# Kernel optimization log

Measured on AMD Instinct MI355X. Metric: run time of the kernel, lower is better.

The kernel has to match this reference:

```python
import jax, jax.numpy as jnp
import numpy as np

HIDDEN = 1024
HEADS = 16
D_HEAD = HIDDEN // HEADS  # 64
N = 2048


def setup_inputs() -> dict:
    key = jax.random.key(0)
    ks = jax.random.split(key, 12)
    s = 1.0 / np.sqrt(HIDDEN)
    return {
        "q": jax.random.normal(ks[0], (N, HIDDEN), jnp.float32),
        "k": jax.random.normal(ks[1], (N, HIDDEN), jnp.float32),
        "v": jax.random.normal(ks[2], (N, HIDDEN), jnp.float32),
        "attn_bias": jax.random.normal(ks[3], (HEADS, 1, N, N), jnp.float32),
        "Wq": jax.random.normal(ks[4], (HIDDEN, HIDDEN), jnp.float32) * s,
        "bq": jax.random.normal(ks[5], (HIDDEN,), jnp.float32) * s,
        "Wk": jax.random.normal(ks[6], (HIDDEN, HIDDEN), jnp.float32) * s,
        "bk": jax.random.normal(ks[7], (HIDDEN,), jnp.float32) * s,
        "Wv": jax.random.normal(ks[8], (HIDDEN, HIDDEN), jnp.float32) * s,
        "bv": jax.random.normal(ks[9], (HIDDEN,), jnp.float32) * s,
        "Wo": jax.random.normal(ks[10], (HIDDEN, HIDDEN), jnp.float32) * s,
        "bo": jax.random.normal(ks[11], (HIDDEN,), jnp.float32) * s,
    }


def reference(q, k, v, attn_bias, Wq, bq, Wk, bk, Wv, bv, Wo, bo):
    # q,k,v: [N, hidden]; attn_bias: [H, 1, N, N]. Attention runs over the
    # node axis (dim 0 in the torch code), inner seq dim is 1 (squeezed).
    n = q.shape[0]
    scale = D_HEAD ** -0.5
    qh = (q @ Wq.T + bq).reshape(n, HEADS, D_HEAD).transpose(1, 0, 2)  # [H,N,d]
    kh = (k @ Wk.T + bk).reshape(n, HEADS, D_HEAD).transpose(1, 0, 2)  # [H,N,d]
    vh = (v @ Wv.T + bv).reshape(n, HEADS, D_HEAD).transpose(1, 0, 2)  # [H,N,d]
    scores = jnp.einsum('hnd,hmd->hnm', qh * scale, kh) + attn_bias[:, 0]  # [H,N,N]
    attn = jax.nn.softmax(scores, axis=-1)
    ctx = jnp.einsum('hnm,hmd->hnd', attn, vh)            # [H,N,d]
    ctx = ctx.transpose(1, 0, 2).reshape(n, HEADS * D_HEAD)  # [N,hidden]
    return ctx @ Wo.T + bo
```

## Files before the change

### kernel.cpp

```cpp
#include <hip/hip_runtime.h>
#include <type_traits>
#include <utility>

#define NT 2048
#define HD 1024
#define NHEAD 16
#define DHEAD 64
#define LOG2E 1.44269504f

typedef float f32x4 __attribute__((ext_vector_type(4)));
typedef __bf16 b16x8 __attribute__((ext_vector_type(8)));
typedef short s16x8 __attribute__((ext_vector_type(8)));
typedef unsigned short u16x8 __attribute__((ext_vector_type(8)));
typedef unsigned short u16x4 __attribute__((ext_vector_type(4)));

template <typename V, typename = void>
struct mfma_takes : std::false_type {};
template <typename V>
struct mfma_takes<V, std::void_t<decltype(__builtin_amdgcn_mfma_f32_16x16x32_bf16(
                         std::declval<V>(), std::declval<V>(), std::declval<f32x4>(), 0, 0, 0))>>
    : std::true_type {};

template <typename V>
__device__ __forceinline__ f32x4 mfma_impl(V a, V b, f32x4 c) {
  return __builtin_amdgcn_mfma_f32_16x16x32_bf16(a, b, c, 0, 0, 0);
}

__device__ __forceinline__ f32x4 mfma_bf16(u16x8 a, u16x8 b, f32x4 c) {
  using V = typename std::conditional<mfma_takes<b16x8>::value, b16x8, s16x8>::type;
  return mfma_impl<V>(__builtin_bit_cast(V, a), __builtin_bit_cast(V, b), c);
}

__device__ __forceinline__ unsigned short f2bf(float f) {
  unsigned int u = __builtin_bit_cast(unsigned int, f);
  return (unsigned short)((u + 0x7FFFu + ((u >> 16) & 1u)) >> 16);
}

__device__ __forceinline__ void gload16(const unsigned short* g, unsigned short* l) {
  __builtin_amdgcn_global_load_lds(
      (__attribute__((address_space(1))) void*)(void*)(g),
      (__attribute__((address_space(3))) void*)(void*)(l), 16, 0, 0);
}

__global__ __launch_bounds__(256) void cvt_bf16(
    const float* __restrict__ s0, const float* __restrict__ s1, const float* __restrict__ s2,
    const float* __restrict__ s3, const float* __restrict__ s4, const float* __restrict__ s5,
    const float* __restrict__ s6,
    unsigned short* __restrict__ d0, unsigned short* __restrict__ d1, unsigned short* __restrict__ d2,
    unsigned short* __restrict__ d3, unsigned short* __restrict__ d4, unsigned short* __restrict__ d5,
    unsigned short* __restrict__ d6) {
  const int seg = blockIdx.y;
  const float* s;
  unsigned short* d;
  switch (seg) {
    case 0: s = s0; d = d0; break;
    case 1: s = s1; d = d1; break;
    case 2: s = s2; d = d2; break;
    case 3: s = s3; d = d3; break;
    case 4: s = s4; d = d4; break;
    case 5: s = s5; d = d5; break;
    default: s = s6; d = d6; break;
  }
  const int n = (seg < 3) ? NT * HD : HD * HD;
  for (int i = blockIdx.x * 2048 + threadIdx.x * 8; i < n; i += gridDim.x * 2048) {
    f32x4 f0 = *reinterpret_cast<const f32x4*>(&s[i]);
    f32x4 f1 = *reinterpret_cast<const f32x4*>(&s[i + 4]);
    u16x8 o;
#pragma unroll
    for (int e = 0; e < 4; ++e) { o[e] = f2bf(f0[e]); o[e + 4] = f2bf(f1[e]); }
    *reinterpret_cast<u16x8*>(&d[i]) = o;
  }
}

__device__ __forceinline__ void gemm_mainloop(
    const unsigned short* __restrict__ A, const unsigned short* __restrict__ B,
    unsigned short* As, unsigned short* Bs, int n0, int m0, f32x4 acc[4][4]) {
  const int tid = threadIdx.x;
  const int lane = tid & 63;
  const int wr = (tid >> 6) >> 1, wc = (tid >> 6) & 1;
  const int srow = tid >> 3;
  const int scol = (tid & 7) << 3;

  for (int kt = 0; kt < HD; kt += 64) {
    __syncthreads();
#pragma unroll
    for (int i = 0; i < 4; ++i) {
      gload16(&A[(size_t)(n0 + srow + i * 32) * HD + kt + scol], As + i * 2048 + tid * 8);
      gload16(&B[(size_t)(m0 + srow + i * 32) * HD + kt + scol], Bs + i * 2048 + tid * 8);
    }
    __syncthreads();
#pragma unroll
    for (int ks = 0; ks < 2; ++ks) {
      const int kcol = ks * 32 + (lane >> 4) * 8;
      u16x8 a[4], b[4];
#pragma unroll
      for (int i = 0; i < 4; ++i)
        a[i] = *reinterpret_cast<const u16x8*>(&As[(wr * 64 + i * 16 + (lane & 15)) * 64 + kcol]);
#pragma unroll
      for (int j = 0; j < 4; ++j)
        b[j] = *reinterpret_cast<const u16x8*>(&Bs[(wc * 64 + j * 16 + (lane & 15)) * 64 + kcol]);
#pragma unroll
      for (int i = 0; i < 4; ++i)
#pragma unroll
        for (int j = 0; j < 4; ++j)
          acc[i][j] = mfma_bf16(a[i], b[j], acc[i][j]);
    }
  }
}

__global__ __launch_bounds__(256) void proj_gemm(
    const unsigned short* __restrict__ qb, const unsigned short* __restrict__ kb,
    const unsigned short* __restrict__ vb,
    const unsigned short* __restrict__ Wqb, const unsigned short* __restrict__ Wkb,
    const unsigned short* __restrict__ Wvb,
    const float* __restrict__ bq, const float* __restrict__ bk, const float* __restrict__ bv,
    unsigned short* __restrict__ Qh, unsigned short* __restrict__ Kh,
    unsigned short* __restrict__ Vt) {
  const int z = blockIdx.z;
  const unsigned short* A = (z == 0) ? qb : (z == 1) ? kb : vb;
  const unsigned short* B = (z == 0) ? Wqb : (z == 1) ? Wkb : Wvb;
  const float* bias = (z == 0) ? bq : (z == 1) ? bk : bv;

  __shared__ unsigned short As[128 * 64];
  __shared__ unsigned short Bs[128 * 64];

  const int n0 = blockIdx.x * 128;
  const int m0 = blockIdx.y * 128;
  const int tid = threadIdx.x;
  const int lane = tid & 63;
  const int wr = (tid >> 6) >> 1, wc = (tid >> 6) & 1;

  f32x4 acc[4][4] = {};
  gemm_mainloop(A, B, As, Bs, n0, m0, acc);

  const int rgrp = (lane >> 4) * 4;
  const float scale = (z == 0) ? 0.125f * LOG2E : 1.0f;
#pragma unroll
  for (int i = 0; i < 4; ++i) {
    const int nb = n0 + wr * 64 + i * 16 + rgrp;
#pragma unroll
    for (int j = 0; j < 4; ++j) {
      const int m = m0 + wc * 64 + j * 16 + (lane & 15);
      const float bb = bias[m];
      if (z == 2) {
        u16x4 pk;
#pragma unroll
        for (int r = 0; r < 4; ++r) pk[r] = f2bf(acc[i][j][r] + bb);
        *reinterpret_cast<u16x4*>(&Vt[(size_t)m * NT + nb]) = pk;
      } else {
        unsigned short* dst = (z == 0) ? Qh : Kh;
#pragma unroll
        for (int r = 0; r < 4; ++r)
          dst[(size_t)(nb + r) * HD + m] = f2bf((acc[i][j][r] + bb) * scale);
      }
    }
  }
}

__global__ __launch_bounds__(256) void attn_kernel(
    const unsigned short* __restrict__ Qh, const unsigned short* __restrict__ Kh,
    const unsigned short* __restrict__ Vt, const float* __restrict__ bias,
    unsigned short* __restrict__ ctx) {
  const int h = blockIdx.y;
  const int q0 = blockIdx.x * 64;
  const int tid = threadIdx.x;
  const int lane = tid & 63;
  const int wave = tid >> 6;

  __shared__ unsigned short Ks[128][72];
  __shared__ unsigned short Vs[64][136];
  __shared__ unsigned short Ps[4][16][136];

  u16x8 qf[2];
  {
    const int qrow = q0 + wave * 16 + (lane & 15);
    const int db = (lane >> 4) * 8;
    qf[0] = *reinterpret_cast<const u16x8*>(&Qh[(size_t)qrow * HD + h * DHEAD + db]);
    qf[1] = *reinterpret_cast<const u16x8*>(&Qh[(size_t)qrow * HD + h * DHEAD + 32 + db]);
  }

  f32x4 oacc[4] = {};
  float mrun[4], lrun[4];
#pragma unroll
  for (int r = 0; r < 4; ++r) { mrun[r] = -3.0e38f; lrun[r] = 0.f; }

  const float* bias_h = bias + (size_t)h * NT * NT;
  const int qlrow = q0 + wave * 16 + (lane >> 4) * 4;

  const int ksr = tid >> 3, ksc = (tid & 7) << 3;
  const int vsd = tid >> 2, vsc = (tid & 3) << 3;
  const unsigned short* Kbase = Kh + h * DHEAD;
  const unsigned short* Vbase = Vt + (size_t)(h * DHEAD + vsd) * NT;

#pragma unroll
  for (int p = 0; p < 4; ++p)
    *reinterpret_cast<u16x8*>(&Ks[ksr + p * 32][ksc]) =
        *reinterpret_cast<const u16x8*>(&Kbase[(size_t)(ksr + p * 32) * HD + ksc]);
#pragma unroll
  for (int p = 0; p < 4; ++p)
    *reinterpret_cast<u16x8*>(&Vs[vsd][vsc + p * 32]) =
        *reinterpret_cast<const u16x8*>(&Vbase[vsc + p * 32]);
  __syncthreads();

  for (int t = 0; t < NT / 128; ++t) {
    const int kt = t * 128;
    float br[8][4];
    const float* bp = bias_h + (size_t)qlrow * NT + kt + (lane & 15);
#pragma unroll
    for (int j = 0; j < 8; ++j)
#pragma unroll
      for (int r = 0; r < 4; ++r) br[j][r] = bp[(size_t)r * NT + j * 16];

    u16x8 kpre[4], vpre[4];
    const bool more = (t + 1 < NT / 128);
    if (more) {
      const int kt2 = kt + 128;
#pragma unroll
      for (int p = 0; p < 4; ++p)
        kpre[p] = *reinterpret_cast<const u16x8*>(&Kbase[(size_t)(kt2 + ksr + p * 32) * HD + ksc]);
#pragma unroll
      for (int p = 0; p < 4; ++p)
        vpre[p] = *reinterpret_cast<const u16x8*>(&Vbase[kt2 + vsc + p * 32]);
    }

    f32x4 s[8] = {};
#pragma unroll
    for (int ks = 0; ks < 2; ++ks) {
      const int kcol = ks * 32 + (lane >> 4) * 8;
#pragma unroll
      for (int j = 0; j < 8; ++j) {
        u16x8 kf = *reinterpret_cast<const u16x8*>(&Ks[j * 16 + (lane & 15)][kcol]);
        s[j] = mfma_bf16(qf[ks], kf, s[j]);
      }
    }
#pragma unroll
    for (int j = 0; j < 8; ++j)
#pragma unroll
      for (int r = 0; r < 4; ++r) s[j][r] = fmaf(br[j][r], LOG2E, s[j][r]);

    float mnew[4];
#pragma unroll
    for (int r = 0; r < 4; ++r) {
      float mx = s[0][r];
#pragma unroll
      for (int j = 1; j < 8; ++j) mx = fmaxf(mx, s[j][r]);
      mx = fmaxf(mx, __shfl_xor(mx, 1));
      mx = fmaxf(mx, __shfl_xor(mx, 2));
      mx = fmaxf(mx, __shfl_xor(mx, 4));
      mx = fmaxf(mx, __shfl_xor(mx, 8));
      mnew[r] = fmaxf(mrun[r], mx);
    }
#pragma unroll
    for (int r = 0; r < 4; ++r) {
      const float corr = exp2f(mrun[r] - mnew[r]);
      lrun[r] *= corr;
#pragma unroll
      for (int nd = 0; nd < 4; ++nd) oacc[nd][r] *= corr;
      mrun[r] = mnew[r];
    }
    float psum[4] = {0.f, 0.f, 0.f, 0.f};
#pragma unroll
    for (int j = 0; j < 8; ++j)
#pragma unroll
      for (int r = 0; r < 4; ++r) {
        const float p = exp2f(s[j][r] - mrun[r]);
        psum[r] += p;
        Ps[wave][(lane >> 4) * 4 + r][j * 16 + (lane & 15)] = f2bf(p);
      }
#pragma unroll
    for (int r = 0; r < 4; ++r) {
      float tsum = psum[r];
      tsum += __shfl_xor(tsum, 1);
      tsum += __shfl_xor(tsum, 2);
      tsum += __shfl_xor(tsum, 4);
      tsum += __shfl_xor(tsum, 8);
      lrun[r] += tsum;
    }

#pragma unroll
    for (int kk = 0; kk < 4; ++kk) {
      const int kcol = kk * 32 + (lane >> 4) * 8;
      u16x8 pa = *reinterpret_cast<const u16x8*>(&Ps[wave][lane & 15][kcol]);
#pragma unroll
      for (int nd = 0; nd < 4; ++nd) {
        u16x8 vb = *reinterpret_cast<const u16x8*>(&Vs[nd * 16 + (lane & 15)][kcol]);
        oacc[nd] = mfma_bf16(pa, vb, oacc[nd]);
      }
    }
    __syncthreads();
    if (more) {
#pragma unroll
      for (int p = 0; p < 4; ++p)
        *reinterpret_cast<u16x8*>(&Ks[ksr + p * 32][ksc]) = kpre[p];
#pragma unroll
      for (int p = 0; p < 4; ++p)
        *reinterpret_cast<u16x8*>(&Vs[vsd][vsc + p * 32]) = vpre[p];
    }
    __syncthreads();
  }

#pragma unroll
  for (int nd = 0; nd < 4; ++nd) {
#pragma unroll
    for (int r = 0; r < 4; ++r) {
      const float val = oacc[nd][r] / lrun[r];
      ctx[(size_t)(qlrow + r) * HD + h * DHEAD + nd * 16 + (lane & 15)] = f2bf(val);
    }
  }
}

__global__ __launch_bounds__(256) void out_gemm(
    const unsigned short* __restrict__ Ain, const unsigned short* __restrict__ Wob,
    const float* __restrict__ bias, float* __restrict__ out) {
  __shared__ unsigned short As[128 * 64];
  __shared__ unsigned short Bs[128 * 64];

  const int n0 = blockIdx.x * 128;
  const int m0 = blockIdx.y * 128;
  const int tid = threadIdx.x;
  const int lane = tid & 63;
  const int wr = (tid >> 6) >> 1, wc = (tid >> 6) & 1;

  f32x4 acc[4][4] = {};
  gemm_mainloop(Ain, Wob, As, Bs, n0, m0, acc);

  const int rgrp = (lane >> 4) * 4;
#pragma unroll
  for (int i = 0; i < 4; ++i) {
    const int nb = n0 + wr * 64 + i * 16 + rgrp;
#pragma unroll
    for (int j = 0; j < 4; ++j) {
      const int m = m0 + wc * 64 + j * 16 + (lane & 15);
      const float bb = bias[m];
#pragma unroll
      for (int r = 0; r < 4; ++r)
        out[(size_t)(nb + r) * HD + m] = acc[i][j][r] + bb;
    }
  }
}

extern "C" void kernel_launch(void* const* d_in, const int* in_sizes, int n_in,
                              void* d_out, int out_size, void* d_ws, size_t ws_size,
                              hipStream_t stream) {
  const float* q  = (const float*)d_in[0];
  const float* k  = (const float*)d_in[1];
  const float* v  = (const float*)d_in[2];
  const float* ab = (const float*)d_in[3];
  const float* Wq = (const float*)d_in[4];
  const float* bq = (const float*)d_in[5];
  const float* Wk = (const float*)d_in[6];
  const float* bk = (const float*)d_in[7];
  const float* Wv = (const float*)d_in[8];
  const float* bv = (const float*)d_in[9];
  const float* Wo = (const float*)d_in[10];
  const float* bo = (const float*)d_in[11];

  unsigned short* qb  = (unsigned short*)d_ws;
  unsigned short* kb  = qb + (size_t)NT * HD;
  unsigned short* vb  = kb + (size_t)NT * HD;
  unsigned short* Wqb = vb + (size_t)NT * HD;
  unsigned short* Wkb = Wqb + (size_t)HD * HD;
  unsigned short* Wvb = Wkb + (size_t)HD * HD;
  unsigned short* Wob = Wvb + (size_t)HD * HD;
  unsigned short* Qh  = Wob + (size_t)HD * HD;
  unsigned short* Kh  = Qh + (size_t)NT * HD;
  unsigned short* Vt  = Kh + (size_t)NT * HD;
  unsigned short* ctx = Vt + (size_t)NT * HD;

  cvt_bf16<<<dim3(512, 7), 256, 0, stream>>>(q, k, v, Wq, Wk, Wv, Wo,
                                             qb, kb, vb, Wqb, Wkb, Wvb, Wob);
  proj_gemm<<<dim3(NT / 128, HD / 128, 3), 256, 0, stream>>>(
      qb, kb, vb, Wqb, Wkb, Wvb, bq, bk, bv, Qh, Kh, Vt);
  attn_kernel<<<dim3(NT / 64, NHEAD), 256, 0, stream>>>(Qh, Kh, Vt, ab, ctx);
  out_gemm<<<dim3(NT / 128, HD / 128), 256, 0, stream>>>(ctx, Wob, bo, (float*)d_out);
}
```

Measured before the change: 147.4 us.

## Double-buffer GEMM mainloop with 64x128 tiles and XCD-aware block mapping

Shrinks the projection and output GEMM tiles to 64x128 and double-buffers shared memory, so the next K-slice loads while the current one computes and there is one barrier per slice. This doubles block count for better occupancy on the many-CU GPU. Grids are flattened to 1D with remapped indices: the GEMMs group blocks by weight column tile, and attention assigns two heads per XCD so each XCD's L2 reuses the same K/V. Costs are more shared memory per block, and the smaller tiles need more A/B traffic per output.

```diff
diff --git a/kernel.cpp b/kernel.cpp
--- a/kernel.cpp
+++ b/kernel.cpp
@@ -72,39 +72,55 @@
   }
 }
 
-__device__ __forceinline__ void gemm_mainloop(
+__device__ __forceinline__ void gemm64x128(
     const unsigned short* __restrict__ A, const unsigned short* __restrict__ B,
-    unsigned short* As, unsigned short* Bs, int n0, int m0, f32x4 acc[4][4]) {
+    int n0, int m0,
+    unsigned short* As0, unsigned short* As1,
+    unsigned short* Bs0, unsigned short* Bs1, f32x4 acc[2][4]) {
   const int tid = threadIdx.x;
   const int lane = tid & 63;
   const int wr = (tid >> 6) >> 1, wc = (tid >> 6) & 1;
   const int srow = tid >> 3;
   const int scol = (tid & 7) << 3;
 
-  for (int kt = 0; kt < HD; kt += 64) {
-    __syncthreads();
-#pragma unroll
-    for (int i = 0; i < 4; ++i) {
-      gload16(&A[(size_t)(n0 + srow + i * 32) * HD + kt + scol], As + i * 2048 + tid * 8);
-      gload16(&B[(size_t)(m0 + srow + i * 32) * HD + kt + scol], Bs + i * 2048 + tid * 8);
-    }
-    __syncthreads();
+  auto stage = [&](int kt, unsigned short* as, unsigned short* bs) {
+#pragma unroll
+    for (int p = 0; p < 2; ++p)
+      gload16(&A[(size_t)(n0 + p * 32 + srow) * HD + kt + scol], as + p * 2048 + tid * 8);
+#pragma unroll
+    for (int p = 0; p < 4; ++p)
+      gload16(&B[(size_t)(m0 + p * 32 + srow) * HD + kt + scol], bs + p * 2048 + tid * 8);
+  };
+  auto comp = [&](const unsigned short* as, const unsigned short* bs) {
 #pragma unroll
     for (int ks = 0; ks < 2; ++ks) {
       const int kcol = ks * 32 + (lane >> 4) * 8;
-      u16x8 a[4], b[4];
-#pragma unroll
-      for (int i = 0; i < 4; ++i)
-        a[i] = *reinterpret_cast<const u16x8*>(&As[(wr * 64 + i * 16 + (lane & 15)) * 64 + kcol]);
+      u16x8 a[2], b[4];
+#pragma unroll
+      for (int i = 0; i < 2; ++i)
+        a[i] = *reinterpret_cast<const u16x8*>(&as[(wr * 32 + i * 16 + (lane & 15)) * 64 + kcol]);
 #pragma unroll
       for (int j = 0; j < 4; ++j)
-        b[j] = *reinterpret_cast<const u16x8*>(&Bs[(wc * 64 + j * 16 + (lane & 15)) * 64 + kcol]);
-#pragma unroll
-      for (int i = 0; i < 4; ++i)
+        b[j] = *reinterpret_cast<const u16x8*>(&bs[(wc * 64 + j * 16 + (lane & 15)) * 64 + kcol]);
+#pragma unroll
+      for (int i = 0; i < 2; ++i)
 #pragma unroll
         for (int j = 0; j < 4; ++j)
           acc[i][j] = mfma_bf16(a[i], b[j], acc[i][j]);
     }
+  };
+
+  stage(0, As0, Bs0);
+  __syncthreads();
+#pragma unroll 1
+  for (int tt = 0; tt < 8; ++tt) {
+    const int kt = tt * 128;
+    stage(kt + 64, As1, Bs1);
+    comp(As0, Bs0);
+    __syncthreads();
+    if (kt + 128 < HD) stage(kt + 128, As0, Bs0);
+    comp(As1, Bs1);
+    __syncthreads();
   }
 }
 
@@ -116,42 +132,46 @@
     const float* __restrict__ bq, const float* __restrict__ bk, const float* __restrict__ bv,
     unsigned short* __restrict__ Qh, unsigned short* __restrict__ Kh,
     unsigned short* __restrict__ Vt) {
-  const int z = blockIdx.z;
+  const int L = blockIdx.x;
+  const int m = L / 96;
+  const int c = L % 96;
+  const int z = c / 32;
+  const int n = c % 32;
+  const int n0 = n * 64, m0 = m * 128;
+
   const unsigned short* A = (z == 0) ? qb : (z == 1) ? kb : vb;
   const unsigned short* B = (z == 0) ? Wqb : (z == 1) ? Wkb : Wvb;
   const float* bias = (z == 0) ? bq : (z == 1) ? bk : bv;
 
-  __shared__ unsigned short As[128 * 64];
-  __shared__ unsigned short Bs[128 * 64];
-
-  const int n0 = blockIdx.x * 128;
-  const int m0 = blockIdx.y * 128;
+  __shared__ unsigned short As0[64 * 64], As1[64 * 64];
+  __shared__ unsigned short Bs0[128 * 64], Bs1[128 * 64];
+
   const int tid = threadIdx.x;
   const int lane = tid & 63;
   const int wr = (tid >> 6) >> 1, wc = (tid >> 6) & 1;
 
-  f32x4 acc[4][4] = {};
-  gemm_mainloop(A, B, As, Bs, n0, m0, acc);
+  f32x4 acc[2][4] = {};
+  gemm64x128(A, B, n0, m0, As0, As1, Bs0, Bs1, acc);
 
   const int rgrp = (lane >> 4) * 4;
   const float scale = (z == 0) ? 0.125f * LOG2E : 1.0f;
 #pragma unroll
-  for (int i = 0; i < 4; ++i) {
-    const int nb = n0 + wr * 64 + i * 16 + rgrp;
+  for (int i = 0; i < 2; ++i) {
+    const int nb = n0 + wr * 32 + i * 16 + rgrp;
 #pragma unroll
     for (int j = 0; j < 4; ++j) {
-      const int m = m0 + wc * 64 + j * 16 + (lane & 15);
-      const float bb = bias[m];
+      const int mcol = m0 + wc * 64 + j * 16 + (lane & 15);
+      const float bb = bias[mcol];
       if (z == 2) {
         u16x4 pk;
 #pragma unroll
         for (int r = 0; r < 4; ++r) pk[r] = f2bf(acc[i][j][r] + bb);
-        *reinterpret_cast<u16x4*>(&Vt[(size_t)m * NT + nb]) = pk;
+        *reinterpret_cast<u16x4*>(&Vt[(size_t)mcol * NT + nb]) = pk;
       } else {
         unsigned short* dst = (z == 0) ? Qh : Kh;
 #pragma unroll
         for (int r = 0; r < 4; ++r)
-          dst[(size_t)(nb + r) * HD + m] = f2bf((acc[i][j][r] + bb) * scale);
+          dst[(size_t)(nb + r) * HD + mcol] = f2bf((acc[i][j][r] + bb) * scale);
       }
     }
   }
@@ -161,8 +181,10 @@
     const unsigned short* __restrict__ Qh, const unsigned short* __restrict__ Kh,
     const unsigned short* __restrict__ Vt, const float* __restrict__ bias,
     unsigned short* __restrict__ ctx) {
-  const int h = blockIdx.y;
-  const int q0 = blockIdx.x * 64;
+  const int id = blockIdx.x;
+  const int xcd = id & 7, slot = id >> 3;
+  const int h = xcd * 2 + (slot >> 5);
+  const int q0 = (slot & 31) * 64;
   const int tid = threadIdx.x;
   const int lane = tid & 63;
   const int wave = tid >> 6;
@@ -312,29 +334,32 @@
 __global__ __launch_bounds__(256) void out_gemm(
     const unsigned short* __restrict__ Ain, const unsigned short* __restrict__ Wob,
     const float* __restrict__ bias, float* __restrict__ out) {
-  __shared__ unsigned short As[128 * 64];
-  __shared__ unsigned short Bs[128 * 64];
-
-  const int n0 = blockIdx.x * 128;
-  const int m0 = blockIdx.y * 128;
+  const int L = blockIdx.x;
+  const int m = L / 32;
+  const int n = L % 32;
+  const int n0 = n * 64, m0 = m * 128;
+
+  __shared__ unsigned short As0[64 * 64], As1[64 * 64];
+  __shared__ unsigned short Bs0[128 * 64], Bs1[128 * 64];
+
   const int tid = threadIdx.x;
   const int lane = tid & 63;
   const int wr = (tid >> 6) >> 1, wc = (tid >> 6) & 1;
 
-  f32x4 acc[4][4] = {};
-  gemm_mainloop(Ain, Wob, As, Bs, n0, m0, acc);
+  f32x4 acc[2][4] = {};
+  gemm64x128(Ain, Wob, n0, m0, As0, As1, Bs0, Bs1, acc);
 
   const int rgrp = (lane >> 4) * 4;
 #pragma unroll
-  for (int i = 0; i < 4; ++i) {
-    const int nb = n0 + wr * 64 + i * 16 + rgrp;
+  for (int i = 0; i < 2; ++i) {
+    const int nb = n0 + wr * 32 + i * 16 + rgrp;
 #pragma unroll
     for (int j = 0; j < 4; ++j) {
-      const int m = m0 + wc * 64 + j * 16 + (lane & 15);
-      const float bb = bias[m];
+      const int mcol = m0 + wc * 64 + j * 16 + (lane & 15);
+      const float bb = bias[mcol];
 #pragma unroll
       for (int r = 0; r < 4; ++r)
-        out[(size_t)(nb + r) * HD + m] = acc[i][j][r] + bb;
+        out[(size_t)(nb + r) * HD + mcol] = acc[i][j][r] + bb;
     }
   }
 }
@@ -369,8 +394,8 @@
 
   cvt_bf16<<<dim3(512, 7), 256, 0, stream>>>(q, k, v, Wq, Wk, Wv, Wo,
                                              qb, kb, vb, Wqb, Wkb, Wvb, Wob);
-  proj_gemm<<<dim3(NT / 128, HD / 128, 3), 256, 0, stream>>>(
+  proj_gemm<<<dim3(768), 256, 0, stream>>>(
       qb, kb, vb, Wqb, Wkb, Wvb, bq, bk, bv, Qh, Kh, Vt);
-  attn_kernel<<<dim3(NT / 64, NHEAD), 256, 0, stream>>>(Qh, Kh, Vt, ab, ctx);
-  out_gemm<<<dim3(NT / 128, HD / 128), 256, 0, stream>>>(ctx, Wob, bo, (float*)d_out);
-}
+  attn_kernel<<<dim3(512), 256, 0, stream>>>(Qh, Kh, Vt, ab, ctx);
+  out_gemm<<<dim3(256), 256, 0, stream>>>(ctx, Wob, bo, (float*)d_out);
+}
```

Result: faster. 132.3 us (-10.3%).
